# Kernel tuning notes

Measured on AMD Instinct MI355X. Metric: run time of the kernel, lower is better.

The kernel has to match this reference:

```python
import jax, jax.numpy as jnp
import numpy as np

T_FINAL = 1.0
N_STEPS = 8  # fixed dopri5 grid (adaptive controller replaced by fixed steps; per-step tableau math identical)

# Dormand-Prince 5(4) tableau (5th-order solution weights; 7th stage weight is 0 so it is skipped)
A_TAB = (
    (),
    (1.0 / 5.0,),
    (3.0 / 40.0, 9.0 / 40.0),
    (44.0 / 45.0, -56.0 / 15.0, 32.0 / 9.0),
    (19372.0 / 6561.0, -25360.0 / 2187.0, 64448.0 / 6561.0, -212.0 / 729.0),
    (9017.0 / 3168.0, -355.0 / 33.0, 46732.0 / 5247.0, 49.0 / 176.0, -5103.0 / 18656.0),
)
B_TAB = (35.0 / 384.0, 0.0, 500.0 / 1113.0, 125.0 / 192.0, -2187.0 / 6784.0, 11.0 / 84.0)
C_TAB = (0.0, 1.0 / 5.0, 3.0 / 10.0, 4.0 / 5.0, 8.0 / 9.0, 1.0)


def setup_inputs() -> dict:
    key = jax.random.key(0)
    k0, k1, k2, k3 = jax.random.split(key, 4)
    B, D, H = 32768, 64, 256
    y = jax.random.normal(k0, (B, D), jnp.float32)
    # Rademacher probe vector (sampled once per integration in before_int)
    e = jax.random.randint(k1, (B, D), 0, 2).astype(jnp.float32) * 2.0 - 1.0
    W1 = jax.random.normal(k2, (D + 1, H), jnp.float32) / np.sqrt(D + 1).astype(np.float32)
    b1 = jnp.zeros((H,), jnp.float32)
    W2 = jax.random.normal(k3, (H, D), jnp.float32) / np.sqrt(H).astype(np.float32)
    b2 = jnp.zeros((D,), jnp.float32)
    return {"y": y, "e": e, "W1": W1, "b1": b1, "W2": W2, "b2": b2}


def _ode_net(t, z, W1, b1, W2, b2):
    # two-layer tanh MLP with time concatenated: [B, D+1] -> [B, H] -> [B, D]
    tcol = jnp.full((z.shape[0], 1), 1.0, z.dtype) * t
    h = jnp.tanh(jnp.concatenate([z, tcol], axis=1) @ W1 + b1)
    return h @ W2 + b2


def _rhs(t, state, e, params):
    # ODEFunc.forward: dx = ode_net(t, z); dlogp = -Hutchinson divergence e^T (df/dz) e
    z, _ = state
    f = lambda zz: _ode_net(t, zz, *params)
    dz, vjp = jax.vjp(f, z)
    e_dfdz = vjp(e)[0]                                   # e^T J, shape [B, D]
    div = jnp.sum(e_dfdz * e, axis=1, keepdims=True)     # [B, 1]
    return (dz, -div)


def _dopri5_step(t, dt, state, e, params):
    ks = []
    for i in range(6):
        if i == 0:
            yi = state
        else:
            ai = A_TAB[i]
            yi = jax.tree_util.tree_map(
                lambda y_, *kk, ai=ai: y_ + dt * sum(a * k for a, k in zip(ai, kk)),
                state, *ks)
        ks.append(_rhs(t + C_TAB[i] * dt, yi, e, params))
    return jax.tree_util.tree_map(
        lambda y_, *kk: y_ + dt * sum(b * k for b, k in zip(B_TAB, kk)),
        state, *ks)


def reference(y, e, W1, b1, W2, b2):
    params = (W1, b1, W2, b2)
    dt = T_FINAL / N_STEPS
    lp0 = jnp.zeros((y.shape[0], 1), y.dtype)  # integrates dlogp/dt = -divergence from 0

    def body(carry, t):
        return _dopri5_step(t, dt, carry, e, params), None

    ts = jnp.arange(N_STEPS, dtype=y.dtype) * jnp.asarray(dt, y.dtype)
    (z, dlog_pz), _ = jax.lax.scan(body, (y, lp0), ts)
    # standard_normal_logprob(z).sum over features
    log_pz = jnp.sum(-0.5 * np.float32(np.log(2.0 * np.pi)) - 0.5 * z * z, axis=1, keepdims=True)
    log_px = log_pz - dlog_pz
    return z, log_px
```

## Files before the change

kernel.cpp:

```cpp
#include <hip/hip_runtime.h>


typedef __bf16 bf16x8 __attribute__((ext_vector_type(8)));
typedef __bf16 bf16x4 __attribute__((ext_vector_type(4)));
typedef float  f32x4  __attribute__((ext_vector_type(4)));
typedef unsigned int u32;

#define MFMA16(a, b, c) __builtin_amdgcn_mfma_f32_16x16x32_bf16((a), (b), (c), 0, 0, 0)

#define SY_S 76
#define SH_S 268

__device__ __forceinline__ float fast_tanh2(float x2) {
    float e = __builtin_amdgcn_exp2f(x2);
    return 1.0f - 2.0f * __builtin_amdgcn_rcpf(e + 1.0f);
}
__device__ __forceinline__ bf16x8 cvt8(f32x4 a, f32x4 b) {
    bf16x8 r;
#pragma unroll
    for (int i = 0; i < 4; ++i) { r[i] = (__bf16)a[i]; r[4 + i] = (__bf16)b[i]; }
    return r;
}

extern "C" __global__ void __launch_bounds__(256, 2)
cnf_kernel(const float* __restrict__ Yg, const float* __restrict__ Eg,
           const float* __restrict__ W1g, const float* __restrict__ b1g,
           const float* __restrict__ W2g, const float* __restrict__ b2g,
           float* __restrict__ Og)
{
    __shared__ __align__(16) __bf16 sYA[16 * SY_S], sYB[16 * SY_S];
    __shared__ __align__(16) __bf16 sHA[16 * SH_S], sHB[16 * SH_S];
    __shared__ float sBW[256];
    __shared__ float sRedSS[128], sRedLP[128];

    const int tid  = threadIdx.x;
    const int wave = tid >> 6;
    const int lane = tid & 63;
    const int quad = lane >> 4;
    const int l16  = lane & 15;
    const int colb = wave * 16;
    const int jb   = wave * 64;
    const int rowA = blockIdx.x * 32 + l16;
    const int rowB = rowA + 16;

    const float TS  = 2.885390081777927f;
    const float IVS = 0.346573590279973f;

    bf16x8 aeA0, aeA1, aeB0, aeB1;
    {
        const float* eA = Eg + rowA * 64;
        const float* eB = Eg + rowB * 64;
        aeA0 = cvt8(*(const f32x4*)(eA + quad * 8),      *(const f32x4*)(eA + quad * 8 + 4));
        aeA1 = cvt8(*(const f32x4*)(eA + 32 + quad * 8), *(const f32x4*)(eA + 32 + quad * 8 + 4));
        aeB0 = cvt8(*(const f32x4*)(eB + quad * 8),      *(const f32x4*)(eB + quad * 8 + 4));
        aeB1 = cvt8(*(const f32x4*)(eB + 32 + quad * 8), *(const f32x4*)(eB + 32 + quad * 8 + 4));
    }

    bf16x8 w1f[8];
#pragma unroll
    for (int t = 0; t < 4; ++t) {
#pragma unroll
        for (int h = 0; h < 2; ++h) {
            const float* src = W1g + (h * 32 + quad * 8) * 256 + jb + t * 16 + l16;
            bf16x8 f;
#pragma unroll
            for (int i = 0; i < 8; ++i) f[i] = (__bf16)(src[i * 256] * TS);
            w1f[t * 2 + h] = f;
        }
    }

    float ghfA[16], ghfB[16];
#pragma unroll
    for (int t = 0; t < 4; ++t) {
        const float* wr = W2g + (jb + t * 16 + l16) * 64;
        bf16x8 aw0 = cvt8(*(const f32x4*)(wr + quad * 8),      *(const f32x4*)(wr + quad * 8 + 4));
        bf16x8 aw1 = cvt8(*(const f32x4*)(wr + 32 + quad * 8), *(const f32x4*)(wr + 32 + quad * 8 + 4));
        f32x4 vA = {0.f,0.f,0.f,0.f}, vB = {0.f,0.f,0.f,0.f};
        f32x4 gA = {0.f,0.f,0.f,0.f}, gB = {0.f,0.f,0.f,0.f};
        vA = MFMA16(w1f[t * 2 + 0], aeA0, vA);  vA = MFMA16(w1f[t * 2 + 1], aeA1, vA);
        vB = MFMA16(w1f[t * 2 + 0], aeB0, vB);  vB = MFMA16(w1f[t * 2 + 1], aeB1, vB);
        gA = MFMA16(aw0, aeA0, gA);             gA = MFMA16(aw1, aeA1, gA);
        gB = MFMA16(aw0, aeB0, gB);             gB = MFMA16(aw1, aeB1, gB);
#pragma unroll
        for (int i = 0; i < 4; ++i) {
            ghfA[t * 4 + i] = gA[i] * vA[i] * IVS;
            ghfB[t * 4 + i] = gB[i] * vB[i] * IVS;
        }
    }

    bf16x8 w2f[8];
#pragma unroll
    for (int c = 0; c < 8; ++c) {
        const float* src = W2g + (c * 32 + quad * 8) * 64 + colb + l16;
        bf16x8 f;
#pragma unroll
        for (int i = 0; i < 8; ++i) f[i] = (__bf16)src[i * 64];
        w2f[c] = f;
    }

    f32x4 zvA = *(const f32x4*)(Yg + rowA * 64 + colb + quad * 4);
    f32x4 zvB = *(const f32x4*)(Yg + rowB * 64 + colb + quad * 4);
    f32x4 bb2 = *(const f32x4*)(b2g + colb + quad * 4);
    const float b1r  = b1g[tid] * TS;
    const float w1tr = W1g[64 * 256 + tid] * TS;

    const float dt = 0.125f;
    float kfA[6][4], kfB[6][4];
    float lppA = 0.f, lppB = 0.f;

#define S0X(arr, g) 0.f
#define S1X(arr, g) (0.2f*arr[0][g])
#define S2X(arr, g) (0.075f*arr[0][g] + 0.225f*arr[1][g])
#define S3X(arr, g) ((44.f/45.f)*arr[0][g] + (-56.f/15.f)*arr[1][g] + (32.f/9.f)*arr[2][g])
#define S4X(arr, g) ((19372.f/6561.f)*arr[0][g] + (-25360.f/2187.f)*arr[1][g] + \
                     (64448.f/6561.f)*arr[2][g] + (-212.f/729.f)*arr[3][g])
#define S5X(arr, g) ((9017.f/3168.f)*arr[0][g] + (-355.f/33.f)*arr[1][g] + \
                     (46732.f/5247.f)*arr[2][g] + (49.f/176.f)*arr[3][g] + \
                     (-5103.f/18656.f)*arr[4][g])
#define CBX(arr, g) ((35.f/384.f)*arr[0][g] + (500.f/1113.f)*arr[2][g] + \
                     (125.f/192.f)*arr[3][g] + (-2187.f/6784.f)*arr[4][g] + \
                     (11.f/84.f)*arr[5][g])

#define MM1T(S, t, DODV) { \
    f32x4 ua = *(const f32x4*)(sBW + jb + (t)*16 + quad * 4); \
    ua = MFMA16(w1f[(t)*2 + 0], a10##S, ua); \
    ua = MFMA16(w1f[(t)*2 + 1], a11##S, ua); \
    float h0 = fast_tanh2(ua[0]), h1 = fast_tanh2(ua[1]); \
    float h2 = fast_tanh2(ua[2]), h3 = fast_tanh2(ua[3]); \
    if (DODV) { \
        dv##S += ghf##S[(t)*4 + 0] * (1.f - h0*h0); \
        dv##S += ghf##S[(t)*4 + 1] * (1.f - h1*h1); \
        dv##S += ghf##S[(t)*4 + 2] * (1.f - h2*h2); \
        dv##S += ghf##S[(t)*4 + 3] * (1.f - h3*h3); \
    } \
    bf16x4 hv; hv[0]=(__bf16)h0; hv[1]=(__bf16)h1; hv[2]=(__bf16)h2; hv[3]=(__bf16)h3; \
    *(bf16x4*)(sH##S + l16 * SH_S + jb + (t)*16 + quad * 4) = hv; }

#define MM2C(S, c, acc) { \
    bf16x8 hf = *(const bf16x8*)(sH##S + l16 * SH_S + (c)*32 + quad * 8); \
    acc = MFMA16(w2f[c], hf, acc); }

#define STAGE(st, CTI, DTB, DODV, SX) { \
    const float ti = t0 + (CTI) * dt; \
    { bf16x4 yv; \
      yv[0] = (__bf16)(zvA[0] + dt * (SX(kfA,0))); \
      yv[1] = (__bf16)(zvA[1] + dt * (SX(kfA,1))); \
      yv[2] = (__bf16)(zvA[2] + dt * (SX(kfA,2))); \
      yv[3] = (__bf16)(zvA[3] + dt * (SX(kfA,3))); \
      *(bf16x4*)(sYA + l16 * SY_S + colb + quad * 4) = yv; } \
    { bf16x4 yv; \
      yv[0] = (__bf16)(zvB[0] + dt * (SX(kfB,0))); \
      yv[1] = (__bf16)(zvB[1] + dt * (SX(kfB,1))); \
      yv[2] = (__bf16)(zvB[2] + dt * (SX(kfB,2))); \
      yv[3] = (__bf16)(zvB[3] + dt * (SX(kfB,3))); \
      *(bf16x4*)(sYB + l16 * SY_S + colb + quad * 4) = yv; } \
    sBW[tid] = b1r + ti * w1tr; \
    __syncthreads();   \
    bf16x8 a10A = *(const bf16x8*)(sYA + l16 * SY_S + quad * 8); \
    bf16x8 a11A = *(const bf16x8*)(sYA + l16 * SY_S + 32 + quad * 8); \
    bf16x8 a10B = *(const bf16x8*)(sYB + l16 * SY_S + quad * 8); \
    bf16x8 a11B = *(const bf16x8*)(sYB + l16 * SY_S + 32 + quad * 8); \
    float dvA = 0.f, dvB = 0.f; \
    MM1T(A,0,DODV) MM1T(B,0,DODV) MM1T(A,1,DODV) MM1T(B,1,DODV) \
    MM1T(A,2,DODV) MM1T(B,2,DODV) MM1T(A,3,DODV) MM1T(B,3,DODV) \
    __syncthreads();   \
    f32x4 faA0 = bb2, faA1 = {0.f,0.f,0.f,0.f}; \
    f32x4 faB0 = bb2, faB1 = {0.f,0.f,0.f,0.f}; \
    MM2C(A,0,faA0) MM2C(B,0,faB0) MM2C(A,1,faA1) MM2C(B,1,faB1) \
    MM2C(A,2,faA0) MM2C(B,2,faB0) MM2C(A,3,faA1) MM2C(B,3,faB1) \
    MM2C(A,4,faA0) MM2C(B,4,faB0) MM2C(A,5,faA1) MM2C(B,5,faB1) \
    MM2C(A,6,faA0) MM2C(B,6,faB0) MM2C(A,7,faA1) MM2C(B,7,faB1) \
    f32x4 faA = faA0 + faA1, faB = faB0 + faB1; \
    kfA[st][0] = faA[0]; kfA[st][1] = faA[1]; kfA[st][2] = faA[2]; kfA[st][3] = faA[3]; \
    kfB[st][0] = faB[0]; kfB[st][1] = faB[1]; kfB[st][2] = faB[2]; kfB[st][3] = faB[3]; \
    if (DODV) { lppA -= (DTB) * dvA; lppB -= (DTB) * dvB; } }

    for (int step = 0; step < 8; ++step) {
        const float t0 = dt * (float)step;
        STAGE(0, 0.f,     dt*(35.f/384.f),    1, S0X)
        STAGE(1, 0.2f,    0.f,                0, S1X)
        STAGE(2, 0.3f,    dt*(500.f/1113.f),  1, S2X)
        STAGE(3, 0.8f,    dt*(125.f/192.f),   1, S3X)
        STAGE(4, 8.f/9.f, dt*(-2187.f/6784.f),1, S4X)
        STAGE(5, 1.f,     dt*(11.f/84.f),     1, S5X)
        zvA[0] += dt * CBX(kfA,0);  zvA[1] += dt * CBX(kfA,1);
        zvA[2] += dt * CBX(kfA,2);  zvA[3] += dt * CBX(kfA,3);
        zvB[0] += dt * CBX(kfB,0);  zvB[1] += dt * CBX(kfB,1);
        zvB[2] += dt * CBX(kfB,2);  zvB[3] += dt * CBX(kfB,3);
    }

    *(f32x4*)(Og + rowA * 64 + colb + quad * 4) = zvA;
    *(f32x4*)(Og + rowB * 64 + colb + quad * 4) = zvB;
    float ssA = zvA[0]*zvA[0] + zvA[1]*zvA[1] + zvA[2]*zvA[2] + zvA[3]*zvA[3];
    float ssB = zvB[0]*zvB[0] + zvB[1]*zvB[1] + zvB[2]*zvB[2] + zvB[3]*zvB[3];
    ssA += __shfl_xor(ssA, 16);  ssA += __shfl_xor(ssA, 32);
    ssB += __shfl_xor(ssB, 16);  ssB += __shfl_xor(ssB, 32);
    float lpA = lppA;  lpA += __shfl_xor(lpA, 16);  lpA += __shfl_xor(lpA, 32);
    float lpB = lppB;  lpB += __shfl_xor(lpB, 16);  lpB += __shfl_xor(lpB, 32);
    if (quad == 0) {
        sRedSS[wave * 16 + l16] = ssA;       sRedLP[wave * 16 + l16] = lpA;
        sRedSS[64 + wave * 16 + l16] = ssB;  sRedLP[64 + wave * 16 + l16] = lpB;
    }
    __syncthreads();
    if (tid < 32) {
        const float CLOG = -58.8120661f;
        int half = tid >> 4, r = tid & 15, base = half * 64;
        float sfull = sRedSS[base + r] + sRedSS[base + 16 + r]
                    + sRedSS[base + 32 + r] + sRedSS[base + 48 + r];
        float lfull = sRedLP[base + r] + sRedLP[base + 16 + r]
                    + sRedLP[base + 32 + r] + sRedLP[base + 48 + r];
        Og[32768 * 64 + blockIdx.x * 32 + half * 16 + r] = CLOG - 0.5f * sfull - lfull;
    }
}

extern "C" void kernel_launch(void* const* d_in, const int* in_sizes, int n_in,
                              void* d_out, int out_size, void* d_ws, size_t ws_size,
                              hipStream_t stream) {
    const float* Yg  = (const float*)d_in[0];
    const float* Eg  = (const float*)d_in[1];
    const float* W1g = (const float*)d_in[2];
    const float* b1g = (const float*)d_in[3];
    const float* W2g = (const float*)d_in[4];
    const float* b2g = (const float*)d_in[5];
    float* Og = (float*)d_out;
    cnf_kernel<<<dim3(1024), dim3(256), 0, stream>>>(Yg, Eg, W1g, b1g, W2g, b2g, Og);
}
```

Before: 249.5 us.

## Precompute per-stage bias table and delay barrier via per-wave chunk rotation

Moves the time-dependent first-layer bias for all 48 stages into a precomputed shared-memory table filled once per block. This removes the per-stage bias write and its hazard on the first barrier. It also rotates each wave's W2 chunk order so every wave starts the second GEMM on the hidden columns it wrote itself, which lets the second barrier move after those first chunks. The aim is less time stalled at barriers, at the cost of about 48KB more LDS per block, which may squeeze occupancy.

Result: no change. 250.1 us (+0.2%).

```diff
diff --git a/kernel.cpp b/kernel.cpp
--- a/kernel.cpp
+++ b/kernel.cpp
@@ -28,9 +28,9 @@
            const float* __restrict__ W2g, const float* __restrict__ b2g,
            float* __restrict__ Og)
 {
+    __shared__ float sBWT[48 * 256];
     __shared__ __align__(16) __bf16 sYA[16 * SY_S], sYB[16 * SY_S];
     __shared__ __align__(16) __bf16 sHA[16 * SH_S], sHB[16 * SH_S];
-    __shared__ float sBW[256];
     __shared__ float sRedSS[128], sRedLP[128];
 
     const int tid  = threadIdx.x;
@@ -45,6 +45,19 @@
 
     const float TS  = 2.885390081777927f;
     const float IVS = 0.346573590279973f;
+    const float dt  = 0.125f;
+
+    {
+        const float b1r  = b1g[tid] * TS;
+        const float w1tr = W1g[64 * 256 + tid] * TS;
+        const float ctis[6] = {0.f, 0.2f, 0.3f, 0.8f, 8.f/9.f, 1.f};
+#pragma unroll
+        for (int st = 0; st < 6; ++st)
+#pragma unroll
+            for (int step = 0; step < 8; ++step)
+                sBWT[(step * 6 + st) * 256 + tid] =
+                    b1r + (dt * ((float)step + ctis[st])) * w1tr;
+    }
 
     bf16x8 aeA0, aeA1, aeB0, aeB1;
     {
@@ -89,22 +102,22 @@
     }
 
     bf16x8 w2f[8];
-#pragma unroll
-    for (int c = 0; c < 8; ++c) {
+    int cofs[8];
+#pragma unroll
+    for (int m = 0; m < 8; ++m) {
+        const int c = (2 * wave + m) & 7;
+        cofs[m] = c * 32;
         const float* src = W2g + (c * 32 + quad * 8) * 64 + colb + l16;
         bf16x8 f;
 #pragma unroll
         for (int i = 0; i < 8; ++i) f[i] = (__bf16)src[i * 64];
-        w2f[c] = f;
+        w2f[m] = f;
     }
 
     f32x4 zvA = *(const f32x4*)(Yg + rowA * 64 + colb + quad * 4);
     f32x4 zvB = *(const f32x4*)(Yg + rowB * 64 + colb + quad * 4);
     f32x4 bb2 = *(const f32x4*)(b2g + colb + quad * 4);
-    const float b1r  = b1g[tid] * TS;
-    const float w1tr = W1g[64 * 256 + tid] * TS;
-
-    const float dt = 0.125f;
+
     float kfA[6][4], kfB[6][4];
     float lppA = 0.f, lppB = 0.f;
 
@@ -121,27 +134,40 @@
                      (125.f/192.f)*arr[3][g] + (-2187.f/6784.f)*arr[4][g] + \
                      (11.f/84.f)*arr[5][g])
 
-#define MM1T(S, t, DODV) { \
-    f32x4 ua = *(const f32x4*)(sBW + jb + (t)*16 + quad * 4); \
-    ua = MFMA16(w1f[(t)*2 + 0], a10##S, ua); \
-    ua = MFMA16(w1f[(t)*2 + 1], a11##S, ua); \
-    float h0 = fast_tanh2(ua[0]), h1 = fast_tanh2(ua[1]); \
-    float h2 = fast_tanh2(ua[2]), h3 = fast_tanh2(ua[3]); \
-    if (DODV) { \
-        dv##S += ghf##S[(t)*4 + 0] * (1.f - h0*h0); \
-        dv##S += ghf##S[(t)*4 + 1] * (1.f - h1*h1); \
-        dv##S += ghf##S[(t)*4 + 2] * (1.f - h2*h2); \
-        dv##S += ghf##S[(t)*4 + 3] * (1.f - h3*h3); \
-    } \
-    bf16x4 hv; hv[0]=(__bf16)h0; hv[1]=(__bf16)h1; hv[2]=(__bf16)h2; hv[3]=(__bf16)h3; \
-    *(bf16x4*)(sH##S + l16 * SH_S + jb + (t)*16 + quad * 4) = hv; }
-
-#define MM2C(S, c, acc) { \
-    bf16x8 hf = *(const bf16x8*)(sH##S + l16 * SH_S + (c)*32 + quad * 8); \
-    acc = MFMA16(w2f[c], hf, acc); }
-
-#define STAGE(st, CTI, DTB, DODV, SX) { \
-    const float ti = t0 + (CTI) * dt; \
+#define MM1P(t, DODV) { \
+    f32x4 bw = *(const f32x4*)(bwR + jb + (t)*16 + quad * 4); \
+    { f32x4 ua = bw; \
+      ua = MFMA16(w1f[(t)*2 + 0], a10A, ua); \
+      ua = MFMA16(w1f[(t)*2 + 1], a11A, ua); \
+      float h0 = fast_tanh2(ua[0]), h1 = fast_tanh2(ua[1]); \
+      float h2 = fast_tanh2(ua[2]), h3 = fast_tanh2(ua[3]); \
+      if (DODV) { \
+          dvA += ghfA[(t)*4 + 0] * (1.f - h0*h0); \
+          dvA += ghfA[(t)*4 + 1] * (1.f - h1*h1); \
+          dvA += ghfA[(t)*4 + 2] * (1.f - h2*h2); \
+          dvA += ghfA[(t)*4 + 3] * (1.f - h3*h3); \
+      } \
+      bf16x4 hv; hv[0]=(__bf16)h0; hv[1]=(__bf16)h1; hv[2]=(__bf16)h2; hv[3]=(__bf16)h3; \
+      *(bf16x4*)(sHA + l16 * SH_S + jb + (t)*16 + quad * 4) = hv; } \
+    { f32x4 ua = bw; \
+      ua = MFMA16(w1f[(t)*2 + 0], a10B, ua); \
+      ua = MFMA16(w1f[(t)*2 + 1], a11B, ua); \
+      float h0 = fast_tanh2(ua[0]), h1 = fast_tanh2(ua[1]); \
+      float h2 = fast_tanh2(ua[2]), h3 = fast_tanh2(ua[3]); \
+      if (DODV) { \
+          dvB += ghfB[(t)*4 + 0] * (1.f - h0*h0); \
+          dvB += ghfB[(t)*4 + 1] * (1.f - h1*h1); \
+          dvB += ghfB[(t)*4 + 2] * (1.f - h2*h2); \
+          dvB += ghfB[(t)*4 + 3] * (1.f - h3*h3); \
+      } \
+      bf16x4 hv; hv[0]=(__bf16)h0; hv[1]=(__bf16)h1; hv[2]=(__bf16)h2; hv[3]=(__bf16)h3; \
+      *(bf16x4*)(sHB + l16 * SH_S + jb + (t)*16 + quad * 4) = hv; } }
+
+#define MM2C(S, m, acc) { \
+    bf16x8 hf = *(const bf16x8*)(sH##S + l16 * SH_S + cofs[m] + quad * 8); \
+    acc = MFMA16(w2f[m], hf, acc); }
+
+#define STAGE(st, DTB, DODV, SX) { \
     { bf16x4 yv; \
       yv[0] = (__bf16)(zvA[0] + dt * (SX(kfA,0))); \
       yv[1] = (__bf16)(zvA[1] + dt * (SX(kfA,1))); \
@@ -154,19 +180,19 @@
       yv[2] = (__bf16)(zvB[2] + dt * (SX(kfB,2))); \
       yv[3] = (__bf16)(zvB[3] + dt * (SX(kfB,3))); \
       *(bf16x4*)(sYB + l16 * SY_S + colb + quad * 4) = yv; } \
-    sBW[tid] = b1r + ti * w1tr; \
     __syncthreads();   \
+    const float* bwR = sBWT + (step * 6 + (st)) * 256; \
     bf16x8 a10A = *(const bf16x8*)(sYA + l16 * SY_S + quad * 8); \
     bf16x8 a11A = *(const bf16x8*)(sYA + l16 * SY_S + 32 + quad * 8); \
     bf16x8 a10B = *(const bf16x8*)(sYB + l16 * SY_S + quad * 8); \
     bf16x8 a11B = *(const bf16x8*)(sYB + l16 * SY_S + 32 + quad * 8); \
     float dvA = 0.f, dvB = 0.f; \
-    MM1T(A,0,DODV) MM1T(B,0,DODV) MM1T(A,1,DODV) MM1T(B,1,DODV) \
-    MM1T(A,2,DODV) MM1T(B,2,DODV) MM1T(A,3,DODV) MM1T(B,3,DODV) \
-    __syncthreads();   \
+    MM1P(0, DODV) MM1P(1, DODV) MM1P(2, DODV) MM1P(3, DODV) \
+     \
     f32x4 faA0 = bb2, faA1 = {0.f,0.f,0.f,0.f}; \
     f32x4 faB0 = bb2, faB1 = {0.f,0.f,0.f,0.f}; \
     MM2C(A,0,faA0) MM2C(B,0,faB0) MM2C(A,1,faA1) MM2C(B,1,faB1) \
+    __syncthreads();   \
     MM2C(A,2,faA0) MM2C(B,2,faB0) MM2C(A,3,faA1) MM2C(B,3,faB1) \
     MM2C(A,4,faA0) MM2C(B,4,faB0) MM2C(A,5,faA1) MM2C(B,5,faB1) \
     MM2C(A,6,faA0) MM2C(B,6,faB0) MM2C(A,7,faA1) MM2C(B,7,faB1) \
@@ -176,13 +202,12 @@
     if (DODV) { lppA -= (DTB) * dvA; lppB -= (DTB) * dvB; } }
 
     for (int step = 0; step < 8; ++step) {
-        const float t0 = dt * (float)step;
-        STAGE(0, 0.f,     dt*(35.f/384.f),    1, S0X)
-        STAGE(1, 0.2f,    0.f,                0, S1X)
-        STAGE(2, 0.3f,    dt*(500.f/1113.f),  1, S2X)
-        STAGE(3, 0.8f,    dt*(125.f/192.f),   1, S3X)
-        STAGE(4, 8.f/9.f, dt*(-2187.f/6784.f),1, S4X)
-        STAGE(5, 1.f,     dt*(11.f/84.f),     1, S5X)
+        STAGE(0, dt*(35.f/384.f),    1, S0X)
+        STAGE(1, 0.f,                0, S1X)
+        STAGE(2, dt*(500.f/1113.f),  1, S2X)
+        STAGE(3, dt*(125.f/192.f),   1, S3X)
+        STAGE(4, dt*(-2187.f/6784.f),1, S4X)
+        STAGE(5, dt*(11.f/84.f),     1, S5X)
         zvA[0] += dt * CBX(kfA,0);  zvA[1] += dt * CBX(kfA,1);
         zvA[2] += dt * CBX(kfA,2);  zvA[3] += dt * CBX(kfA,3);
         zvB[0] += dt * CBX(kfB,0);  zvB[1] += dt * CBX(kfB,1);
```
